# Kernel optimization log

Hardware: AMD Instinct MI355X
Metric: run time of the kernel (lower is better)

## Reference

```python
import jax, jax.numpy as jnp
import numpy as np
from functools import partial

DN = ('NCHW', 'OIHW', 'NCHW')


def dwise_conv(x, pw, dw):
    # pointwise 1x1 conv then depthwise 3x3 conv (pad 1), no bias
    c = pw.shape[0]
    h = jax.lax.conv_general_dilated(x, pw, (1, 1), 'VALID', dimension_numbers=DN)
    return jax.lax.conv_general_dilated(h, dw, (1, 1), ((1, 1), (1, 1)),
                                        dimension_numbers=DN, feature_group_count=c)


def l2norm(t, eps=1e-12):
    # torch F.normalize(dim=-1): x / max(||x||_2, eps)
    n = jnp.sqrt(jnp.sum(t * t, axis=-1, keepdims=True))
    return t / jnp.maximum(n, eps)


def cross_attention(x, y, z, temperature, q_pw, q_dw, k_pw, k_dw, v_pw, v_dw, proj_w, num_heads=3):
    b, c, h, w = x.shape
    hc = c // num_heads  # per-head channels
    q = x + dwise_conv(x, q_pw, q_dw)
    k = y + dwise_conv(y, k_pw, k_dw)
    v = z + dwise_conv(z, v_pw, v_dw)
    # b (head hc) h w -> b head hc (h w)
    q = q.reshape(b, num_heads, hc, h * w)
    k = k.reshape(b, num_heads, hc, h * w)
    v = v.reshape(b, num_heads, hc, h * w)
    q = l2norm(q)
    k = l2norm(k)
    # transposed attention: small hc x hc score per head
    attn = jnp.einsum('bhcn,bhdn->bhcd', q, k) * temperature  # temperature broadcasts (head,1,1)
    attn = jax.nn.softmax(attn, axis=-1)
    out = jnp.einsum('bhcd,bhdn->bhcn', attn, v)
    out = out.reshape(b, c, h, w)
    return jax.lax.conv_general_dilated(out, proj_w, (1, 1), 'VALID', dimension_numbers=DN)


def setup_inputs() -> dict:
    key = jax.random.key(0)
    ks = jax.random.split(key, 12)
    B, C, H, W, HEADS = 8, 96, 192, 192, 3
    s = 0.05
    return {
        'x': jax.random.normal(ks[0], (B, C, H, W), jnp.float32),
        'y': jax.random.normal(ks[1], (B, C, H, W), jnp.float32),
        'z': jax.random.normal(ks[2], (B, C, H, W), jnp.float32),
        'temperature': jnp.ones((HEADS, 1, 1), jnp.float32),
        'q_pw': jax.random.normal(ks[3], (C, C, 1, 1), jnp.float32) * s,
        'q_dw': jax.random.normal(ks[4], (C, 1, 3, 3), jnp.float32) * s,
        'k_pw': jax.random.normal(ks[5], (C, C, 1, 1), jnp.float32) * s,
        'k_dw': jax.random.normal(ks[6], (C, 1, 3, 3), jnp.float32) * s,
        'v_pw': jax.random.normal(ks[7], (C, C, 1, 1), jnp.float32) * s,
        'v_dw': jax.random.normal(ks[8], (C, 1, 3, 3), jnp.float32) * s,
        'proj_w': jax.random.normal(ks[9], (C, C, 1, 1), jnp.float32) * s,
    }


def reference(x, y, z, temperature, q_pw, q_dw, k_pw, k_dw, v_pw, v_dw, proj_w):
    return cross_attention(x, y, z, temperature, q_pw, q_dw, k_pw, k_dw, v_pw, v_dw, proj_w, num_heads=3)
```

## Files before the change

### kernel.cpp

```cpp
#include <hip/hip_runtime.h>


#define B_  8
#define C_  96
#define W_  192
#define HW_ 36864
#define NB_ 32

typedef __attribute__((ext_vector_type(8)))  short short8;
typedef __attribute__((ext_vector_type(4)))  float f32x4;
typedef __attribute__((ext_vector_type(16))) float f32x16;

__device__ __forceinline__ unsigned short f2b(float f){
  unsigned u = __float_as_uint(f);
  u += 0x7fffu + ((u >> 16) & 1u);
  return (unsigned short)(u >> 16);
}
__device__ __forceinline__ float blo(unsigned u){ return __uint_as_float(u << 16); }
__device__ __forceinline__ float bhi(unsigned u){ return __uint_as_float(u & 0xffff0000u); }

__device__ __forceinline__ void barrier_lds(){
  asm volatile("s_waitcnt lgkmcnt(0)\n\ts_barrier" ::: "memory");
}

__global__ __launch_bounds__(768, 1)
void k_conv_all(const float* __restrict__ x0, const float* __restrict__ x1,
                const float* __restrict__ x2,
                const float* __restrict__ pw0, const float* __restrict__ pw1,
                const float* __restrict__ pw2,
                const float* __restrict__ dw0, const float* __restrict__ dw1,
                const float* __restrict__ dw2,
                unsigned short* __restrict__ o0, unsigned short* __restrict__ o1,
                unsigned short* __restrict__ o2,
                float* __restrict__ n0, float* __restrict__ n1)
{
  __shared__ unsigned short xrow[192 * 104];
  __shared__ unsigned short hring[3][96 * 196];

  const int t = threadIdx.x, lane = t & 63, wv = t >> 6;
  const int band = blockIdx.x, b = blockIdx.y, cid = blockIdx.z;
  const float* xsrc = (cid == 0) ? x0 : (cid == 1) ? x1 : x2;
  const float* pw   = (cid == 0) ? pw0 : (cid == 1) ? pw1 : pw2;
  const float* dwt  = (cid == 0) ? dw0 : (cid == 1) ? dw1 : dw2;
  unsigned short* outq = (cid == 0) ? o0 : (cid == 1) ? o1 : o2;
  float* nrm = (cid == 0) ? n0 : (cid == 1) ? n1 : nullptr;

  const int r0 = band * 6;
  const int l15 = lane & 15, l4 = lane >> 4;
  const int mtg = wv % 6, ntg = wv / 6;
  const float* xb = xsrc + (size_t)b * C_ * HW_;

  int scp[3], spg[3];
  #pragma unroll
  for (int i = 0; i < 3; ++i){
    const int idx = i * 768 + t;
    scp[i] = idx / 48; spg[i] = idx - scp[i] * 48;
  }

  short8 afrag[3];
  #pragma unroll
  for (int ks = 0; ks < 3; ++ks){
    const int m = mtg * 16 + l15;
    const float* ap = pw + m * 96 + ks * 32 + l4 * 8;
    const float4 f0 = *(const float4*)ap;
    const float4 f1 = *(const float4*)(ap + 4);
    union { short8 v; unsigned short u[8]; } tmp;
    tmp.u[0]=f2b(f0.x); tmp.u[1]=f2b(f0.y); tmp.u[2]=f2b(f0.z); tmp.u[3]=f2b(f0.w);
    tmp.u[4]=f2b(f1.x); tmp.u[5]=f2b(f1.y); tmp.u[6]=f2b(f1.z); tmp.u[7]=f2b(f1.w);
    afrag[ks] = tmp.v;
  }

  {
    uint4* p = (uint4*)&hring[0][0];
    for (int i = t; i < 7056; i += 768) p[i] = make_uint4(0,0,0,0);
  }

  float ssq[8];
  #pragma unroll
  for (int i = 0; i < 8; ++i) ssq[i] = 0.f;

  auto stage_write = [&](const float4* fa, const float4* fb){
    #pragma unroll
    for (int i = 0; i < 3; ++i){
      const int pg = spg[i];
      const unsigned pk0 = (unsigned)f2b(fa[i].x) | ((unsigned)f2b(fb[i].x) << 16);
      const unsigned pk1 = (unsigned)f2b(fa[i].y) | ((unsigned)f2b(fb[i].y) << 16);
      const unsigned pk2 = (unsigned)f2b(fa[i].z) | ((unsigned)f2b(fb[i].z) << 16);
      const unsigned pk3 = (unsigned)f2b(fa[i].w) | ((unsigned)f2b(fb[i].w) << 16);
      const int s = (pg >> 1) & 3;
      const unsigned a0 = (s & 1) ? pk1 : pk0;
      const unsigned a1 = (s & 1) ? pk0 : pk1;
      const unsigned a2 = (s & 1) ? pk3 : pk2;
      const unsigned a3 = (s & 1) ? pk2 : pk3;
      const unsigned q0 = (s & 2) ? a2 : a0;
      const unsigned q1 = (s & 2) ? a3 : a1;
      const unsigned q2 = (s & 2) ? a0 : a2;
      const unsigned q3 = (s & 2) ? a1 : a3;
      unsigned short* basep = xrow + (4*pg) * 104 + 2*scp[i];
      *(unsigned*)(basep + ((0 ^ s) * 104)) = q0;
      *(unsigned*)(basep + ((1 ^ s) * 104)) = q1;
      *(unsigned*)(basep + ((2 ^ s) * 104)) = q2;
      *(unsigned*)(basep + ((3 ^ s) * 104)) = q3;
    }
  };
  auto stage_load = [&](int rs, float4* fa, float4* fb){
    #pragma unroll
    for (int i = 0; i < 3; ++i){
      const float* xp = xb + (size_t)(2*scp[i]) * HW_ + (size_t)rs * W_ + 4*spg[i];
      fa[i] = *(const float4*)xp;
      fb[i] = *(const float4*)(xp + HW_);
    }
  };

  if (r0 - 1 >= 0){
    float4 fa[3], fb[3];
    stage_load(r0 - 1, fa, fb);
    stage_write(fa, fb);
  }
  barrier_lds();

  #pragma unroll 1
  for (int r = r0 - 1; r <= r0 + 6; ++r){
    const int slot = (r + 3) % 3;
    const int rs = r + 1;
    const bool do_stage = (rs <= r0 + 6) && (rs < 192);
    float4 sfa[3], sfb[3];
    if (do_stage) stage_load(rs, sfa, sfb);

    if (r >= 0 && r < 192){
      f32x4 acc[6];
      #pragma unroll
      for (int nt = 0; nt < 6; ++nt){
        acc[nt][0]=0.f; acc[nt][1]=0.f; acc[nt][2]=0.f; acc[nt][3]=0.f;
      }
      #pragma unroll
      for (int ks = 0; ks < 3; ++ks){
        #pragma unroll
        for (int nt = 0; nt < 6; ++nt){
          const short8 bv = *(const short8*)(xrow + (ntg*96 + nt*16 + l15) * 104 + ks*32 + l4*8);
          acc[nt] = __builtin_amdgcn_mfma_f32_16x16x32_bf16(afrag[ks], bv, acc[nt], 0, 0, 0);
        }
      }
      unsigned short* hs = &hring[slot][0];
      #pragma unroll
      for (int nt = 0; nt < 6; ++nt)
        #pragma unroll
        for (int reg = 0; reg < 4; ++reg){
          const int m = mtg*16 + l4*4 + reg;
          const int n = ntg*96 + nt*16 + l15;
          hs[m * 196 + 1 + n] = f2b(acc[nt][reg]);
        }
    } else {
      uint4* p = (uint4*)&hring[slot][0];
      for (int i = t; i < 2352; i += 768) p[i] = make_uint4(0,0,0,0);
    }
    barrier_lds();

    if (do_stage) stage_write(sfa, sfb);
    if (r - 1 >= r0){
      const int rr = r - 1;
      const unsigned short* h0 = &hring[(rr + 2) % 3][0];
      const unsigned short* h1 = &hring[(rr + 3) % 3][0];
      const unsigned short* h2 = &hring[(rr + 4) % 3][0];
      if (lane < 48){
        const int g = lane;
        float4 xr_[8];
        const float* xrp = xb + (size_t)rr * W_ + 4*g;
        #pragma unroll
        for (int cc = 0; cc < 8; ++cc)
          xr_[cc] = *(const float4*)(xrp + (size_t)(wv * 8 + cc) * HW_);
        #pragma unroll
        for (int cc = 0; cc < 8; ++cc){
          const int chs = __builtin_amdgcn_readfirstlane(wv * 8 + cc);
          float wgt[9];
          #pragma unroll
          for (int i = 0; i < 9; ++i) wgt[i] = dwt[chs * 9 + i];
          const int rb = chs * 196 + 4 * g;
          float hv[3][6];
          {
            const unsigned short* hp[3] = {h0 + rb, h1 + rb, h2 + rb};
            #pragma unroll
            for (int d = 0; d < 3; ++d){
              const uint2 ua = *(const uint2*)(hp[d]);
              const unsigned ub = *(const unsigned*)(hp[d] + 4);
              hv[d][0]=blo(ua.x); hv[d][1]=bhi(ua.x); hv[d][2]=blo(ua.y);
              hv[d][3]=bhi(ua.y); hv[d][4]=blo(ub);   hv[d][5]=bhi(ub);
            }
          }
          float o[4] = {xr_[cc].x, xr_[cc].y, xr_[cc].z, xr_[cc].w};
          #pragma unroll
          for (int j = 0; j < 4; ++j){
            float s = o[j];
            #pragma unroll
            for (int d = 0; d < 3; ++d){
              s = fmaf(wgt[d*3+0], hv[d][j],   s);
              s = fmaf(wgt[d*3+1], hv[d][j+1], s);
              s = fmaf(wgt[d*3+2], hv[d][j+2], s);
            }
            o[j] = s;
            ssq[cc] = fmaf(s, s, ssq[cc]);
          }
          const size_t cb = (size_t)(b * C_ + chs) * HW_ + (size_t)rr * W_ + 4*g;
          const unsigned p0 = (unsigned)f2b(o[0]) | ((unsigned)f2b(o[1]) << 16);
          const unsigned p1 = (unsigned)f2b(o[2]) | ((unsigned)f2b(o[3]) << 16);
          *(uint2*)(outq + cb) = make_uint2(p0, p1);
        }
      }
    }
    barrier_lds();
  }

  if (nrm){
    #pragma unroll
    for (int cc = 0; cc < 8; ++cc){
      float s = ssq[cc];
      #pragma unroll
      for (int off = 32; off; off >>= 1) s += __shfl_xor(s, off);
      if (lane == 0)
        nrm[((size_t)b * NB_ + band) * C_ + wv * 8 + cc] = s;
    }
  }
}

__global__ __launch_bounds__(256, 2)
void k_gemm(const unsigned short* __restrict__ Bsrc, const float* __restrict__ Asrc,
            float* __restrict__ Dst)
{
  __shared__ unsigned short xT[256 * 104];
  __shared__ unsigned short aw[96 * 104];
  const int t = threadIdx.x;
  const int b = blockIdx.y;
  const int p0 = blockIdx.x * 256;
  const int lane = t & 63, w = t >> 6;
  const int l15 = lane & 15, l4 = lane >> 4;

  const float* Ab = Asrc + b * C_ * C_;
  #pragma unroll
  for (int j = 0; j < 18; ++j){
    const int pi = j * 256 + t;
    const int row = pi / 48, c2 = (pi - row * 48) * 2;
    const float a0 = Ab[row * 96 + c2], a1 = Ab[row * 96 + c2 + 1];
    *(unsigned*)(aw + row * 104 + c2) = (unsigned)f2b(a0) | ((unsigned)f2b(a1) << 16);
  }
  #pragma unroll 1
  for (int i = 0; i < 12; ++i){
    const int idx = i * 256 + t;
    const int cp = idx >> 6, pg = idx & 63;
    const unsigned short* vp = Bsrc + (size_t)b * C_ * HW_ + (size_t)(2*cp) * HW_ + p0 + 4*pg;
    const uint2 ua = *(const uint2*)vp;
    const uint2 ub = *(const uint2*)(vp + HW_);
    const unsigned pk0 = (ua.x & 0xffffu) | (ub.x << 16);
    const unsigned pk1 = (ua.x >> 16)     | (ub.x & 0xffff0000u);
    const unsigned pk2 = (ua.y & 0xffffu) | (ub.y << 16);
    const unsigned pk3 = (ua.y >> 16)     | (ub.y & 0xffff0000u);
    const int s = (pg >> 1) & 3;
    const unsigned a0 = (s & 1) ? pk1 : pk0;
    const unsigned a1 = (s & 1) ? pk0 : pk1;
    const unsigned a2 = (s & 1) ? pk3 : pk2;
    const unsigned a3 = (s & 1) ? pk2 : pk3;
    const unsigned q0 = (s & 2) ? a2 : a0;
    const unsigned q1 = (s & 2) ? a3 : a1;
    const unsigned q2 = (s & 2) ? a0 : a2;
    const unsigned q3 = (s & 2) ? a1 : a3;
    unsigned short* basep = xT + (4*pg) * 104 + 2*cp;
    *(unsigned*)(basep + ((0 ^ s) * 104)) = q0;
    *(unsigned*)(basep + ((1 ^ s) * 104)) = q1;
    *(unsigned*)(basep + ((2 ^ s) * 104)) = q2;
    *(unsigned*)(basep + ((3 ^ s) * 104)) = q3;
  }
  __syncthreads();

  f32x4 acc[6][4];
  #pragma unroll
  for (int i = 0; i < 6; ++i)
    #pragma unroll
    for (int j = 0; j < 4; ++j){ acc[i][j][0]=0.f; acc[i][j][1]=0.f; acc[i][j][2]=0.f; acc[i][j][3]=0.f; }

  #pragma unroll
  for (int ks = 0; ks < 3; ++ks){
    short8 a[6];
    #pragma unroll
    for (int mt = 0; mt < 6; ++mt)
      a[mt] = *(const short8*)(aw + (mt * 16 + l15) * 104 + ks * 32 + l4 * 8);
    #pragma unroll
    for (int nt = 0; nt < 4; ++nt){
      const short8 bv = *(const short8*)(xT + (w * 64 + nt * 16 + l15) * 104 + ks * 32 + l4 * 8);
      #pragma unroll
      for (int mt = 0; mt < 6; ++mt)
        acc[mt][nt] = __builtin_amdgcn_mfma_f32_16x16x32_bf16(a[mt], bv, acc[mt][nt], 0, 0, 0);
    }
  }

  float* D = Dst + (size_t)b * C_ * HW_ + p0;
  #pragma unroll
  for (int mt = 0; mt < 6; ++mt)
    #pragma unroll
    for (int nt = 0; nt < 4; ++nt)
      #pragma unroll
      for (int r = 0; r < 4; ++r)
        D[(size_t)(mt * 16 + l4 * 4 + r) * HW_ + w * 64 + nt * 16 + l15] = acc[mt][nt][r];
}

__global__ __launch_bounds__(256, 2)
void k_gram(const unsigned short* __restrict__ qb, const unsigned short* __restrict__ kb,
            float* __restrict__ Gp)
{
  __shared__ unsigned short pan[2][32 * 520];
  const int t = threadIdx.x, lane = t & 63, w = t >> 6;
  const int ns = blockIdx.x, bh = blockIdx.y;
  const int b = bh / 3, h = bh - b * 3;
  const size_t base = ((size_t)b * C_ + h * 32) * HW_ + ns * 1536;
  const int l31 = lane & 31, l5 = lane >> 5;

  f32x16 acc;
  #pragma unroll
  for (int r = 0; r < 16; ++r) acc[r] = 0.f;

  #pragma unroll 1
  for (int rd = 0; rd < 3; ++rd){
    __syncthreads();
    #pragma unroll 8
    for (int j = 0; j < 64; ++j){
      const int idx = j * 256 + t;
      const int op = idx >> 13;
      const int rem = idx & 8191;
      const int ch = rem >> 8, dcol = rem & 255;
      const unsigned* src = (const unsigned*)((op ? kb : qb) + base + (size_t)ch * HW_ + rd * 512) + dcol;
      *(unsigned*)(&pan[op][ch * 520 + dcol * 2]) = *src;
    }
    __syncthreads();
    #pragma unroll
    for (int j8 = 0; j8 < 8; ++j8){
      const int s = j8 * 4 + w;
      const short8 av = *(const short8*)(&pan[0][l31 * 520 + s * 16 + l5 * 8]);
      const short8 bv = *(const short8*)(&pan[1][l31 * 520 + s * 16 + l5 * 8]);
      acc = __builtin_amdgcn_mfma_f32_32x32x16_bf16(av, bv, acc, 0, 0, 0);
    }
  }
  __syncthreads();
  float* red = (float*)pan;
  #pragma unroll
  for (int r = 0; r < 16; ++r) red[w * 1024 + r * 64 + lane] = acc[r];
  __syncthreads();
  #pragma unroll
  for (int q = 0; q < 4; ++q){
    const int fi = q * 256 + t;
    const float v = red[fi] + red[1024 + fi] + red[2048 + fi] + red[3072 + fi];
    const int rr = fi >> 6, ll = fi & 63;
    const int c = (rr & 3) + 8 * (rr >> 2) + 4 * (ll >> 5);
    const int d = ll & 31;
    Gp[(((size_t)ns * 24 + bh) * 32 + c) * 32 + d] = v;
  }
}

__global__ __launch_bounds__(256)
void k_attn(const float* __restrict__ Gp, const float* __restrict__ qqp,
            const float* __restrict__ kkp, const float* __restrict__ temp,
            const float* __restrict__ proj, float* __restrict__ M)
{
  const int b = blockIdx.x, t = threadIdx.x;
  __shared__ float at[3][32][32];
  __shared__ float ninv[2][C_];
  if (t < 2 * C_){
    const int kind = t / C_, r = t - kind * C_;
    const float* P = kind ? kkp : qqp;
    float s = 0.f;
    #pragma unroll
    for (int ns = 0; ns < NB_; ++ns) s += P[((size_t)b * NB_ + ns) * C_ + r];
    ninv[kind][r] = 1.f / fmaxf(sqrtf(s), 1e-12f);
  }
  __syncthreads();
  for (int idx = t; idx < 3 * 1024; idx += 256){
    const int h = idx >> 10, rem = idx & 1023, cc = rem >> 5, dd = rem & 31;
    float g = 0.f;
    #pragma unroll
    for (int ns = 0; ns < 24; ++ns)
      g += Gp[(((size_t)ns * 24 + b * 3 + h) * 32 + cc) * 32 + dd];
    at[h][cc][dd] = g * ninv[0][h * 32 + cc] * ninv[1][h * 32 + dd] * temp[h];
  }
  __syncthreads();
  if (t < C_){
    const int h = t >> 5, cc = t & 31;
    float m = -1e30f;
    for (int dd = 0; dd < 32; ++dd) m = fmaxf(m, at[h][cc][dd]);
    float s = 0.f;
    for (int dd = 0; dd < 32; ++dd){ const float e = expf(at[h][cc][dd] - m); at[h][cc][dd] = e; s += e; }
    const float inv = 1.f / s;
    for (int dd = 0; dd < 32; ++dd) at[h][cc][dd] *= inv;
  }
  __syncthreads();
  for (int idx = t; idx < C_ * C_; idx += 256){
    const int o = idx / 96, hd = idx - o * 96, h = hd >> 5, dd = hd & 31;
    float m = 0.f;
    #pragma unroll
    for (int cc = 0; cc < 32; ++cc)
      m = fmaf(proj[o * 96 + h * 32 + cc], at[h][cc][dd], m);
    M[(size_t)b * 9216 + idx] = m;
  }
}

extern "C" void kernel_launch(void* const* d_in, const int* in_sizes, int n_in,
                              void* d_out, int out_size, void* d_ws, size_t ws_size,
                              hipStream_t stream)
{
  const float* x     = (const float*)d_in[0];
  const float* y     = (const float*)d_in[1];
  const float* z     = (const float*)d_in[2];
  const float* temp  = (const float*)d_in[3];
  const float* q_pwc = (const float*)d_in[4];
  const float* q_dwc = (const float*)d_in[5];
  const float* k_pwc = (const float*)d_in[6];
  const float* k_dwc = (const float*)d_in[7];
  const float* v_pwc = (const float*)d_in[8];
  const float* v_dwc = (const float*)d_in[9];
  const float* proj  = (const float*)d_in[10];

  char* ws = (char*)d_ws;
  unsigned short* qb = (unsigned short*)(ws + 56623104);
  unsigned short* kb = (unsigned short*)(ws + 113246208);
  unsigned short* vb = (unsigned short*)(ws + 169869312);
  float* qqp = (float*)(ws + 226492416);
  float* kkp = (float*)(ws + 226590720);
  float* Gp  = (float*)(ws + 4194304);
  float* M   = (float*)(ws + 8388608);
  float* out = (float*)d_out;

  k_conv_all<<<dim3(NB_, B_, 3), 768, 0, stream>>>(
      x, y, z, q_pwc, k_pwc, v_pwc, q_dwc, k_dwc, v_dwc, qb, kb, vb, qqp, kkp);
  k_gram<<<dim3(24, 24), 256, 0, stream>>>(qb, kb, Gp);
  k_attn<<<B_, 256, 0, stream>>>(Gp, qqp, kkp, temp, proj, M);
  k_gemm<<<dim3(HW_ / 256, B_), 256, 0, stream>>>(vb, M, out);
}
```

Measured before the change: 281.5 us.

## Double-buffer conv staging and keep depthwise row window in registers

Splits the x staging tile into two buffers and shrinks the pointwise-output ring to two slots. Each lane now keeps the two previous pointwise rows in registers as a rolling window, so the depthwise stage reads only one new row from LDS per iteration instead of three. This lets the mid-iteration barrier be removed: the depthwise pass now runs one row behind, and the loop gains one extra iteration. The aim is to cut LDS traffic and synchronisation inside the banded fused conv kernel. The cost is 48 extra registers per thread at 768 threads per block, and double-buffered staging that uses more LDS for xrow.

```diff
diff --git a/kernel.cpp b/kernel.cpp
--- a/kernel.cpp
+++ b/kernel.cpp
@@ -34,8 +34,8 @@
                 unsigned short* __restrict__ o2,
                 float* __restrict__ n0, float* __restrict__ n1)
 {
-  __shared__ unsigned short xrow[192 * 104];
-  __shared__ unsigned short hring[3][96 * 196];
+  __shared__ unsigned short xrow[2][192 * 104];
+  __shared__ unsigned short hring[2][96 * 196];
 
   const int t = threadIdx.x, lane = t & 63, wv = t >> 6;
   const int band = blockIdx.x, b = blockIdx.y, cid = blockIdx.z;
@@ -72,14 +72,26 @@
 
   {
     uint4* p = (uint4*)&hring[0][0];
-    for (int i = t; i < 7056; i += 768) p[i] = make_uint4(0,0,0,0);
+    for (int i = t; i < 4704; i += 768) p[i] = make_uint4(0,0,0,0);
   }
 
   float ssq[8];
   #pragma unroll
   for (int i = 0; i < 8; ++i) ssq[i] = 0.f;
 
-  auto stage_write = [&](const float4* fa, const float4* fb){
+  unsigned h0lo[8], h0hi[8], h0ex[8];
+  unsigned h1lo[8], h1hi[8], h1ex[8];
+
+  auto stage_load = [&](int rs, float4* fa, float4* fb){
+    #pragma unroll
+    for (int i = 0; i < 3; ++i){
+      const float* xp = xb + (size_t)(2*scp[i]) * HW_ + (size_t)rs * W_ + 4*spg[i];
+      fa[i] = *(const float4*)xp;
+      fb[i] = *(const float4*)(xp + HW_);
+    }
+  };
+  auto stage_write = [&](int buf, const float4* fa, const float4* fb){
+    unsigned short* xw = &xrow[buf][0];
     #pragma unroll
     for (int i = 0; i < 3; ++i){
       const int pg = spg[i];
@@ -96,114 +108,117 @@
       const unsigned q1 = (s & 2) ? a3 : a1;
       const unsigned q2 = (s & 2) ? a0 : a2;
       const unsigned q3 = (s & 2) ? a1 : a3;
-      unsigned short* basep = xrow + (4*pg) * 104 + 2*scp[i];
+      unsigned short* basep = xw + (4*pg) * 104 + 2*scp[i];
       *(unsigned*)(basep + ((0 ^ s) * 104)) = q0;
       *(unsigned*)(basep + ((1 ^ s) * 104)) = q1;
       *(unsigned*)(basep + ((2 ^ s) * 104)) = q2;
       *(unsigned*)(basep + ((3 ^ s) * 104)) = q3;
     }
   };
-  auto stage_load = [&](int rs, float4* fa, float4* fb){
-    #pragma unroll
-    for (int i = 0; i < 3; ++i){
-      const float* xp = xb + (size_t)(2*scp[i]) * HW_ + (size_t)rs * W_ + 4*spg[i];
-      fa[i] = *(const float4*)xp;
-      fb[i] = *(const float4*)(xp + HW_);
-    }
-  };
 
   if (r0 - 1 >= 0){
     float4 fa[3], fb[3];
     stage_load(r0 - 1, fa, fb);
-    stage_write(fa, fb);
+    stage_write((r0 + 3) & 1, fa, fb);
   }
   barrier_lds();
 
   #pragma unroll 1
-  for (int r = r0 - 1; r <= r0 + 6; ++r){
-    const int slot = (r + 3) % 3;
+  for (int r = r0 - 1; r <= r0 + 7; ++r){
+    const int slr = (r + 4) & 1;
     const int rs = r + 1;
     const bool do_stage = (rs <= r0 + 6) && (rs < 192);
     float4 sfa[3], sfb[3];
     if (do_stage) stage_load(rs, sfa, sfb);
 
-    if (r >= 0 && r < 192){
-      f32x4 acc[6];
-      #pragma unroll
-      for (int nt = 0; nt < 6; ++nt){
-        acc[nt][0]=0.f; acc[nt][1]=0.f; acc[nt][2]=0.f; acc[nt][3]=0.f;
-      }
-      #pragma unroll
-      for (int ks = 0; ks < 3; ++ks){
+    if (r <= r0 + 6){
+      if (r >= 0 && r < 192){
+        const unsigned short* xr = &xrow[slr][0];
+        f32x4 acc[6];
         #pragma unroll
         for (int nt = 0; nt < 6; ++nt){
-          const short8 bv = *(const short8*)(xrow + (ntg*96 + nt*16 + l15) * 104 + ks*32 + l4*8);
-          acc[nt] = __builtin_amdgcn_mfma_f32_16x16x32_bf16(afrag[ks], bv, acc[nt], 0, 0, 0);
+          acc[nt][0]=0.f; acc[nt][1]=0.f; acc[nt][2]=0.f; acc[nt][3]=0.f;
         }
+        #pragma unroll
+        for (int ks = 0; ks < 3; ++ks){
+          #pragma unroll
+          for (int nt = 0; nt < 6; ++nt){
+            const short8 bv = *(const short8*)(xr + (ntg*96 + nt*16 + l15) * 104 + ks*32 + l4*8);
+            acc[nt] = __builtin_amdgcn_mfma_f32_16x16x32_bf16(afrag[ks], bv, acc[nt], 0, 0, 0);
+          }
+        }
+        unsigned short* hs = &hring[slr][0];
+        #pragma unroll
+        for (int nt = 0; nt < 6; ++nt)
+          #pragma unroll
+          for (int reg = 0; reg < 4; ++reg){
+            const int m = mtg*16 + l4*4 + reg;
+            const int n = ntg*96 + nt*16 + l15;
+            hs[m * 196 + 1 + n] = f2b(acc[nt][reg]);
+          }
+      } else {
+        uint4* p = (uint4*)&hring[slr][0];
+        for (int i = t; i < 2352; i += 768) p[i] = make_uint4(0,0,0,0);
       }
-      unsigned short* hs = &hring[slot][0];
-      #pragma unroll
-      for (int nt = 0; nt < 6; ++nt)
-        #pragma unroll
-        for (int reg = 0; reg < 4; ++reg){
-          const int m = mtg*16 + l4*4 + reg;
-          const int n = ntg*96 + nt*16 + l15;
-          hs[m * 196 + 1 + n] = f2b(acc[nt][reg]);
-        }
-    } else {
-      uint4* p = (uint4*)&hring[slot][0];
-      for (int i = t; i < 2352; i += 768) p[i] = make_uint4(0,0,0,0);
-    }
-    barrier_lds();
-
-    if (do_stage) stage_write(sfa, sfb);
-    if (r - 1 >= r0){
-      const int rr = r - 1;
-      const unsigned short* h0 = &hring[(rr + 2) % 3][0];
-      const unsigned short* h1 = &hring[(rr + 3) % 3][0];
-      const unsigned short* h2 = &hring[(rr + 4) % 3][0];
+    }
+
+    if (do_stage) stage_write(slr ^ 1, sfa, sfb);
+
+    if (r >= r0){
+      unsigned nlo[8], nhi[8], nex[8];
       if (lane < 48){
         const int g = lane;
-        float4 xr_[8];
-        const float* xrp = xb + (size_t)rr * W_ + 4*g;
-        #pragma unroll
-        for (int cc = 0; cc < 8; ++cc)
-          xr_[cc] = *(const float4*)(xrp + (size_t)(wv * 8 + cc) * HW_);
+        const unsigned short* hb_ = &hring[slr ^ 1][0];
         #pragma unroll
         for (int cc = 0; cc < 8; ++cc){
-          const int chs = __builtin_amdgcn_readfirstlane(wv * 8 + cc);
-          float wgt[9];
+          const unsigned short* hp = hb_ + (wv*8 + cc) * 196 + 4*g;
+          const uint2 ua = *(const uint2*)hp;
+          nlo[cc] = ua.x; nhi[cc] = ua.y;
+          nex[cc] = *(const unsigned*)(hp + 4);
+        }
+        if (r >= r0 + 2){
+          const int rr = r - 2;
+          float4 xr_[8];
+          const float* xrp = xb + (size_t)rr * W_ + 4*g;
           #pragma unroll
-          for (int i = 0; i < 9; ++i) wgt[i] = dwt[chs * 9 + i];
-          const int rb = chs * 196 + 4 * g;
-          float hv[3][6];
-          {
-            const unsigned short* hp[3] = {h0 + rb, h1 + rb, h2 + rb};
+          for (int cc = 0; cc < 8; ++cc)
+            xr_[cc] = *(const float4*)(xrp + (size_t)(wv*8 + cc) * HW_);
+          #pragma unroll
+          for (int cc = 0; cc < 8; ++cc){
+            const int chs = __builtin_amdgcn_readfirstlane(wv*8 + cc);
+            float wgt[9];
             #pragma unroll
-            for (int d = 0; d < 3; ++d){
-              const uint2 ua = *(const uint2*)(hp[d]);
-              const unsigned ub = *(const unsigned*)(hp[d] + 4);
-              hv[d][0]=blo(ua.x); hv[d][1]=bhi(ua.x); hv[d][2]=blo(ua.y);
-              hv[d][3]=bhi(ua.y); hv[d][4]=blo(ub);   hv[d][5]=bhi(ub);
+            for (int i = 0; i < 9; ++i) wgt[i] = dwt[chs * 9 + i];
+            float hv[3][6];
+            hv[0][0]=blo(h0lo[cc]); hv[0][1]=bhi(h0lo[cc]); hv[0][2]=blo(h0hi[cc]);
+            hv[0][3]=bhi(h0hi[cc]); hv[0][4]=blo(h0ex[cc]); hv[0][5]=bhi(h0ex[cc]);
+            hv[1][0]=blo(h1lo[cc]); hv[1][1]=bhi(h1lo[cc]); hv[1][2]=blo(h1hi[cc]);
+            hv[1][3]=bhi(h1hi[cc]); hv[1][4]=blo(h1ex[cc]); hv[1][5]=bhi(h1ex[cc]);
+            hv[2][0]=blo(nlo[cc]);  hv[2][1]=bhi(nlo[cc]);  hv[2][2]=blo(nhi[cc]);
+            hv[2][3]=bhi(nhi[cc]);  hv[2][4]=blo(nex[cc]);  hv[2][5]=bhi(nex[cc]);
+            float o[4] = {xr_[cc].x, xr_[cc].y, xr_[cc].z, xr_[cc].w};
+            #pragma unroll
+            for (int j = 0; j < 4; ++j){
+              float s = o[j];
+              #pragma unroll
+              for (int d = 0; d < 3; ++d){
+                s = fmaf(wgt[d*3+0], hv[d][j],   s);
+                s = fmaf(wgt[d*3+1], hv[d][j+1], s);
+                s = fmaf(wgt[d*3+2], hv[d][j+2], s);
+              }
+              o[j] = s;
+              ssq[cc] = fmaf(s, s, ssq[cc]);
             }
+            const size_t cb = (size_t)(b * C_ + chs) * HW_ + (size_t)rr * W_ + 4*g;
+            const unsigned p0 = (unsigned)f2b(o[0]) | ((unsigned)f2b(o[1]) << 16);
+            const unsigned p1 = (unsigned)f2b(o[2]) | ((unsigned)f2b(o[3]) << 16);
+            *(uint2*)(outq + cb) = make_uint2(p0, p1);
           }
-          float o[4] = {xr_[cc].x, xr_[cc].y, xr_[cc].z, xr_[cc].w};
-          #pragma unroll
-          for (int j = 0; j < 4; ++j){
-            float s = o[j];
-            #pragma unroll
-            for (int d = 0; d < 3; ++d){
-              s = fmaf(wgt[d*3+0], hv[d][j],   s);
-              s = fmaf(wgt[d*3+1], hv[d][j+1], s);
-              s = fmaf(wgt[d*3+2], hv[d][j+2], s);
-            }
-            o[j] = s;
-            ssq[cc] = fmaf(s, s, ssq[cc]);
-          }
-          const size_t cb = (size_t)(b * C_ + chs) * HW_ + (size_t)rr * W_ + 4*g;
-          const unsigned p0 = (unsigned)f2b(o[0]) | ((unsigned)f2b(o[1]) << 16);
-          const unsigned p1 = (unsigned)f2b(o[2]) | ((unsigned)f2b(o[3]) << 16);
-          *(uint2*)(outq + cb) = make_uint2(p0, p1);
+        }
+        #pragma unroll
+        for (int cc = 0; cc < 8; ++cc){
+          h0lo[cc]=h1lo[cc]; h0hi[cc]=h1hi[cc]; h0ex[cc]=h1ex[cc];
+          h1lo[cc]=nlo[cc];  h1hi[cc]=nhi[cc];  h1ex[cc]=nex[cc];
         }
       }
     }
```

Measured after the change: 421.5 us. 49.7% more time.
